# Performance work log

Measured on AMD Instinct MI355X. Metric: run time of the kernel, lower is better.

## Reference

```python
import jax, jax.numpy as jnp
import numpy as np

N_HEAD = 16
RMS_EPS = 1.1920928955078125e-07  # torch float32 finfo eps (F.rms_norm default)


def _apply_rotary(x, cos, sin):
    # x: [B,T,H,D], cos/sin: [1,T,1,D/2]
    d = x.shape[-1] // 2
    x1, x2 = x[..., :d], x[..., d:]
    return jnp.concatenate([x1 * cos + x2 * sin, -x1 * sin + x2 * cos], axis=-1)


def _rms_norm(x):
    var = jnp.mean(jnp.square(x), axis=-1, keepdims=True)
    return x * jax.lax.rsqrt(var + RMS_EPS)


def setup_inputs() -> dict:
    key = jax.random.key(0)
    ks = jax.random.split(key, 5)
    B, T, C, H = 2, 2048, 1024, N_HEAD
    D = C // H
    x = jax.random.normal(ks[0], (B, T, C), dtype=jnp.float32)
    cos = jax.random.uniform(ks[1], (1, T, 1, D // 2), dtype=jnp.float32)
    sin = jax.random.uniform(ks[2], (1, T, 1, D // 2), dtype=jnp.float32)
    kv_w = jax.random.normal(ks[3], (C, C), dtype=jnp.float32) * (C ** -0.5)
    proj_w = jax.random.normal(ks[4], (C, C), dtype=jnp.float32) * (C ** -0.5)
    return {"x": x, "cos": cos, "sin": sin, "kv_w": kv_w, "proj_w": proj_w, "window_left": 1024}


def reference(x, cos, sin, kv_w, proj_w, window_left):
    B, T, C = x.shape
    H = N_HEAD
    D = C // H
    scale = D ** -0.5

    q = x.reshape(B, T, H, D)                       # no Q projection
    kv = (x @ kv_w.T).reshape(B, T, H, D)           # tied K=V projection

    q = _rms_norm(_apply_rotary(q, cos, sin))
    kv = _rms_norm(_apply_rotary(kv, cos, sin))

    # scores: [B,H,T,T]
    scores = jnp.einsum('bqhd,bkhd->bhqk', q, kv) * scale

    pos = jnp.arange(T)
    dist = pos[:, None] - pos[None, :]              # query_pos - key_pos
    allowed = (dist >= 0) & (dist <= window_left)   # causal + sliding window
    scores = jnp.where(allowed[None, None], scores, -jnp.inf)

    attn = jax.nn.softmax(scores, axis=-1)
    out = jnp.einsum('bhqk,bkhd->bqhd', attn, kv).reshape(B, T, C)
    return out @ proj_w.T
```

## Files before the change

### kernel.cpp

```cpp
#include <hip/hip_runtime.h>
#include <hip/hip_bf16.h>

using u16 = unsigned short;
typedef __attribute__((ext_vector_type(8))) short short8v;
typedef __attribute__((ext_vector_type(4))) float f32x4;

#define MFMA16(a, b, c) __builtin_amdgcn_mfma_f32_16x16x32_bf16((a), (b), (c), 0, 0, 0)

#define GLOAD16(g, l) __builtin_amdgcn_global_load_lds(                       \
    (const __attribute__((address_space(1))) void*)(const void*)(g),          \
    (__attribute__((address_space(3))) void*)(void*)(l), 16, 0, 0)

static __device__ __forceinline__ u16 f2bf(float x) {
  __hip_bfloat16 h = __float2bfloat16(x);
  return __builtin_bit_cast(u16, h);
}

__global__ __launch_bounds__(256) void cast_f32_bf16(const float* __restrict__ s,
                                                     u16* __restrict__ d, int n) {
  int i = (blockIdx.x * 256 + threadIdx.x) * 4;
  if (i >= n) return;
  float4 v = *reinterpret_cast<const float4*>(s + i);
  ushort4 o;
  o.x = f2bf(v.x); o.y = f2bf(v.y); o.z = f2bf(v.z); o.w = f2bf(v.w);
  *reinterpret_cast<ushort4*>(d + i) = o;
}

__global__ __launch_bounds__(256) void gemm_bt(const u16* __restrict__ A,
                                               const u16* __restrict__ Bt,
                                               float* __restrict__ C,
                                               int M, int N, int K) {
  __shared__ u16 As[2][64 * 32];
  __shared__ u16 Bs[2][128 * 32];
  unsigned flat = blockIdx.y * gridDim.x + blockIdx.x;
  unsigned nwg = gridDim.x * gridDim.y;
  unsigned swz = (flat & 7) * (nwg >> 3) + (flat >> 3);
  int bm = swz % gridDim.x, bn = swz / gridDim.x;
  int tid = threadIdx.x;
  int wid = tid >> 6, l = tid & 63, lr = l & 15, lg = l >> 4;
  int wr = wid >> 1, wc = wid & 1;

  int srow = l >> 2, scol = (l & 3) * 8;
  const u16* Ag  = A  + (size_t)(bm * 64 + wid * 16 + srow) * K + scol;
  const u16* Bg0 = Bt + (size_t)(bn * 128 + wid * 32 + srow) * K + scol;
  const u16* Bg1 = Bg0 + (size_t)16 * K;

  f32x4 acc[2][4];
#pragma unroll
  for (int m = 0; m < 2; m++)
#pragma unroll
    for (int n = 0; n < 4; n++) acc[m][n] = (f32x4){0.f, 0.f, 0.f, 0.f};

  GLOAD16(Ag, &As[0][wid * 512]);
  GLOAD16(Bg0, &Bs[0][wid * 1024]);
  GLOAD16(Bg1, &Bs[0][wid * 1024 + 512]);
  __syncthreads();

  int cur = 0;
  for (int k0 = 0; k0 < K; k0 += 32) {
    if (k0 + 32 < K) {
      int nb = cur ^ 1;
      GLOAD16(Ag + k0 + 32, &As[nb][wid * 512]);
      GLOAD16(Bg0 + k0 + 32, &Bs[nb][wid * 1024]);
      GLOAD16(Bg1 + k0 + 32, &Bs[nb][wid * 1024 + 512]);
    }

    short8v af[2], bfr[4];
#pragma unroll
    for (int m = 0; m < 2; m++)
      af[m] = *reinterpret_cast<const short8v*>(&As[cur][(wr * 32 + m * 16 + lr) * 32 + lg * 8]);
#pragma unroll
    for (int n = 0; n < 4; n++)
      bfr[n] = *reinterpret_cast<const short8v*>(&Bs[cur][(wc * 64 + n * 16 + lr) * 32 + lg * 8]);
#pragma unroll
    for (int m = 0; m < 2; m++)
#pragma unroll
      for (int n = 0; n < 4; n++) acc[m][n] = MFMA16(af[m], bfr[n], acc[m][n]);

    __syncthreads();
    cur ^= 1;
  }

#pragma unroll
  for (int m = 0; m < 2; m++)
#pragma unroll
    for (int n = 0; n < 4; n++)
#pragma unroll
      for (int r = 0; r < 4; r++) {
        int row = bm * 64 + wr * 32 + m * 16 + lg * 4 + r;
        int col = bn * 128 + wc * 64 + n * 16 + lr;
        C[(size_t)row * N + col] = acc[m][n][r];
      }
}

__global__ __launch_bounds__(256) void rope_rms(const float* __restrict__ src,
                                                u16* __restrict__ dst,
                                                const float* __restrict__ cosp,
                                                const float* __restrict__ sinp,
                                                float scale) {
  int R = blockIdx.x * 4 + (threadIdx.x >> 6);
  int l = threadIdx.x & 63;
  int h = R & 15;
  int bt = R >> 4;
  int t = bt & 2047, b = bt >> 11;

  float v = src[((size_t)R << 6) + l];
  float p = __shfl_xor(v, 32);
  float c = cosp[(t << 5) + (l & 31)];
  float s = sinp[(t << 5) + (l & 31)];
  float r = v * c + ((l < 32) ? p * s : -p * s);
  float sq = r * r;
  sq += __shfl_xor(sq, 32);
  sq += __shfl_xor(sq, 16);
  sq += __shfl_xor(sq, 8);
  sq += __shfl_xor(sq, 4);
  sq += __shfl_xor(sq, 2);
  sq += __shfl_xor(sq, 1);
  float inv = rsqrtf(sq * (1.0f / 64.0f) + 1.1920928955078125e-07f) * scale;
  dst[((((size_t)b * 16 + h) * 2048 + t) << 6) + l] = f2bf(r * inv);
}

__global__ __launch_bounds__(256) void transpose_td(const u16* __restrict__ src,
                                                    u16* __restrict__ dst) {
  __shared__ u16 Ld[64][72];
  int t0 = blockIdx.x << 6, bh = blockIdx.y;
  int tid = threadIdx.x;
#pragma unroll
  for (int i = 0; i < 2; i++) {
    int c = tid + i * 256, tr = c >> 3, sg = c & 7;
    *reinterpret_cast<short8v*>(&Ld[tr][sg * 8]) =
        *reinterpret_cast<const short8v*>(src + ((size_t)bh * 2048 + t0 + tr) * 64 + sg * 8);
  }
  __syncthreads();
#pragma unroll
  for (int i = 0; i < 2; i++) {
    int c = tid + i * 256, dr = c >> 3, sg = c & 7;
    short8v v;
#pragma unroll
    for (int j = 0; j < 8; j++) v[j] = (short)Ld[sg * 8 + j][dr];
    *reinterpret_cast<short8v*>(dst + ((size_t)bh * 64 + dr) * 2048 + t0 + sg * 8) = v;
  }
}

__global__ __launch_bounds__(256) void attn_swa(const u16* __restrict__ Q,
                                                const u16* __restrict__ KV,
                                                const u16* __restrict__ KVt,
                                                u16* __restrict__ O,
                                                const int* __restrict__ winp) {
  const int T = 2048;
  int bid = blockIdx.x;
  int bh = bid & 31;
  int qi = 31 - (bid >> 5);
  int q0 = qi << 6;
  int b = bh >> 4, h = bh & 15;
  int W = *winp;
  int tid = threadIdx.x;
  int wid = tid >> 6, l = tid & 63, lr = l & 15, lg = l >> 4;

  __shared__ u16 Kl[64][72];
  __shared__ u16 Vt[64][72];
  __shared__ u16 Pl[4][16][72];

  const u16* Qb = Q + (((size_t)bh * T + q0 + wid * 16 + lr) << 6);
  short8v aq0 = *reinterpret_cast<const short8v*>(Qb + lg * 8);
  short8v aq1 = *reinterpret_cast<const short8v*>(Qb + 32 + lg * 8);

  const short one_bf = (short)0x3F80;
  short8v vones = {one_bf, one_bf, one_bf, one_bf, one_bf, one_bf, one_bf, one_bf};

  float m_run[4], l_run[4];
  f32x4 oacc[4];
#pragma unroll
  for (int r = 0; r < 4; r++) { m_run[r] = -1e30f; l_run[r] = 0.f; }
#pragma unroll
  for (int dt = 0; dt < 4; dt++) oacc[dt] = (f32x4){0.f, 0.f, 0.f, 0.f};

  int lo = q0 - W;
  if (lo < 0) lo = 0;
  lo &= ~63;

  const u16* KVbh  = KV + (((size_t)bh * T) << 6);
  const u16* KVtbh = KVt + ((size_t)bh << 6) * T;
  int r8 = tid >> 3, sg = tid & 7;

  short8v vK0 = *reinterpret_cast<const short8v*>(KVbh + ((size_t)(lo + r8) << 6) + sg * 8);
  short8v vK1 = *reinterpret_cast<const short8v*>(KVbh + ((size_t)(lo + r8 + 32) << 6) + sg * 8);
  short8v vV0 = *reinterpret_cast<const short8v*>(KVtbh + (size_t)r8 * T + lo + sg * 8);
  short8v vV1 = *reinterpret_cast<const short8v*>(KVtbh + (size_t)(r8 + 32) * T + lo + sg * 8);

  for (int kt = lo; kt <= q0; kt += 64) {
    __syncthreads();
    *reinterpret_cast<short8v*>(&Kl[r8][sg * 8]) = vK0;
    *reinterpret_cast<short8v*>(&Kl[r8 + 32][sg * 8]) = vK1;
    *reinterpret_cast<short8v*>(&Vt[r8][sg * 8]) = vV0;
    *reinterpret_cast<short8v*>(&Vt[r8 + 32][sg * 8]) = vV1;
    __syncthreads();
    if (kt < q0) {
      vK0 = *reinterpret_cast<const short8v*>(KVbh + ((size_t)(kt + 64 + r8) << 6) + sg * 8);
      vK1 = *reinterpret_cast<const short8v*>(KVbh + ((size_t)(kt + 64 + r8 + 32) << 6) + sg * 8);
      vV0 = *reinterpret_cast<const short8v*>(KVtbh + (size_t)r8 * T + kt + 64 + sg * 8);
      vV1 = *reinterpret_cast<const short8v*>(KVtbh + (size_t)(r8 + 32) * T + kt + 64 + sg * 8);
    }

    f32x4 s[4];
#pragma unroll
    for (int nt = 0; nt < 4; nt++) {
      s[nt] = (f32x4){0.f, 0.f, 0.f, 0.f};
      short8v b0 = *reinterpret_cast<const short8v*>(&Kl[nt * 16 + lr][lg * 8]);
      s[nt] = MFMA16(aq0, b0, s[nt]);
      short8v b1 = *reinterpret_cast<const short8v*>(&Kl[nt * 16 + lr][32 + lg * 8]);
      s[nt] = MFMA16(aq1, b1, s[nt]);
    }

    bool edge = (kt + 63 > q0 + wid * 16) || ((q0 - kt) + wid * 16 + 15 > W);

    float al4[4];
#pragma unroll
    for (int r = 0; r < 4; r++) {
      float sv[4], mt;
      if (edge) {
        int t = q0 + wid * 16 + lg * 4 + r;
        mt = -3e38f;
#pragma unroll
        for (int nt = 0; nt < 4; nt++) {
          int k = kt + nt * 16 + lr;
          float val = ((k <= t) && (t - k <= W)) ? s[nt][r] : -3e38f;
          sv[nt] = val;
          mt = fmaxf(mt, val);
        }
      } else {
#pragma unroll
        for (int nt = 0; nt < 4; nt++) sv[nt] = s[nt][r];
        mt = fmaxf(fmaxf(sv[0], sv[1]), fmaxf(sv[2], sv[3]));
      }
      mt = fmaxf(mt, __shfl_xor(mt, 1));
      mt = fmaxf(mt, __shfl_xor(mt, 2));
      mt = fmaxf(mt, __shfl_xor(mt, 4));
      mt = fmaxf(mt, __shfl_xor(mt, 8));
      float mn = fmaxf(m_run[r], mt);
      float al = exp2f(m_run[r] - mn);
      m_run[r] = mn;
      al4[r] = al;
#pragma unroll
      for (int nt = 0; nt < 4; nt++) {
        Pl[wid][lg * 4 + r][nt * 16 + lr] = f2bf(exp2f(sv[nt] - mn));
      }
#pragma unroll
      for (int dt = 0; dt < 4; dt++) oacc[dt][r] *= al;
    }

    short8v ap0 = *reinterpret_cast<const short8v*>(&Pl[wid][lr][lg * 8]);
    short8v ap1 = *reinterpret_cast<const short8v*>(&Pl[wid][lr][32 + lg * 8]);
    f32x4 psum = (f32x4){0.f, 0.f, 0.f, 0.f};
    psum = MFMA16(ap0, vones, psum);
    psum = MFMA16(ap1, vones, psum);
#pragma unroll
    for (int dt = 0; dt < 4; dt++) {
      short8v v0 = *reinterpret_cast<const short8v*>(&Vt[dt * 16 + lr][lg * 8]);
      oacc[dt] = MFMA16(ap0, v0, oacc[dt]);
      short8v v1 = *reinterpret_cast<const short8v*>(&Vt[dt * 16 + lr][32 + lg * 8]);
      oacc[dt] = MFMA16(ap1, v1, oacc[dt]);
    }
#pragma unroll
    for (int r = 0; r < 4; r++) l_run[r] = l_run[r] * al4[r] + psum[r];
  }

#pragma unroll
  for (int r = 0; r < 4; r++) {
    int t = q0 + wid * 16 + lg * 4 + r;
    float inv = 1.f / l_run[r];
#pragma unroll
    for (int dt = 0; dt < 4; dt++) {
      O[(((size_t)b * T + t) << 10) + (h << 6) + dt * 16 + lr] = f2bf(oacc[dt][r] * inv);
    }
  }
}

extern "C" void kernel_launch(void* const* d_in, const int* in_sizes, int n_in,
                              void* d_out, int out_size, void* d_ws, size_t ws_size,
                              hipStream_t stream) {
  (void)in_sizes; (void)n_in; (void)out_size; (void)ws_size;
  const float* x    = (const float*)d_in[0];
  const float* cosp = (const float*)d_in[1];
  const float* sinp = (const float*)d_in[2];
  const float* kvw  = (const float*)d_in[3];
  const float* pw   = (const float*)d_in[4];
  const int*   win  = (const int*)d_in[5];

  char* w = (char*)d_ws;
  u16*   xbf   = (u16*)(w);
  u16*   kvwbf = (u16*)(w + (8u << 20));
  u16*   pwbf  = (u16*)(w + (10u << 20));
  float* kvf   = (float*)(w + (12u << 20));
  u16*   kvt   = (u16*)(w + (12u << 20));
  u16*   aout  = (u16*)(w + (20u << 20));
  u16*   kvbf  = (u16*)(w + (28u << 20));
  u16*   qbf   = xbf;

  cast_f32_bf16<<<4096, 256, 0, stream>>>(x, xbf, 4194304);
  cast_f32_bf16<<<1024, 256, 0, stream>>>(kvw, kvwbf, 1048576);
  cast_f32_bf16<<<1024, 256, 0, stream>>>(pw, pwbf, 1048576);

  gemm_bt<<<dim3(64, 8), 256, 0, stream>>>(xbf, kvwbf, kvf, 4096, 1024, 1024);

  rope_rms<<<16384, 256, 0, stream>>>(x, qbf, cosp, sinp, 0.18033688011112042f);
  rope_rms<<<16384, 256, 0, stream>>>(kvf, kvbf, cosp, sinp, 1.0f);

  transpose_td<<<dim3(32, 32), 256, 0, stream>>>(kvbf, kvt);

  attn_swa<<<1024, 256, 0, stream>>>(qbf, kvbf, kvt, aout, win);

  gemm_bt<<<dim3(64, 8), 256, 0, stream>>>(aout, pwbf, (float*)d_out, 4096, 1024, 1024);
}
```

Baseline: 199.5 us.

## Deepen GEMM LDS pipeline, fuse cast launches, add MFMA priority hints

```diff
diff --git a/kernel.cpp b/kernel.cpp
--- a/kernel.cpp
+++ b/kernel.cpp
@@ -16,22 +16,27 @@
   return __builtin_bit_cast(u16, h);
 }
 
-__global__ __launch_bounds__(256) void cast_f32_bf16(const float* __restrict__ s,
-                                                     u16* __restrict__ d, int n) {
-  int i = (blockIdx.x * 256 + threadIdx.x) * 4;
-  if (i >= n) return;
-  float4 v = *reinterpret_cast<const float4*>(s + i);
+__global__ __launch_bounds__(256) void cast3_f32_bf16(const float* __restrict__ a, u16* __restrict__ da,
+                                                      const float* __restrict__ b, u16* __restrict__ db,
+                                                      const float* __restrict__ c, u16* __restrict__ dc) {
+  int bid = blockIdx.x;
+  const float* s; u16* d; int i;
+  if (bid < 4096)      { s = a; d = da; i = bid; }
+  else if (bid < 5120) { s = b; d = db; i = bid - 4096; }
+  else                 { s = c; d = dc; i = bid - 5120; }
+  int idx = (i * 256 + threadIdx.x) * 4;
+  float4 v = *reinterpret_cast<const float4*>(s + idx);
   ushort4 o;
   o.x = f2bf(v.x); o.y = f2bf(v.y); o.z = f2bf(v.z); o.w = f2bf(v.w);
-  *reinterpret_cast<ushort4*>(d + i) = o;
+  *reinterpret_cast<ushort4*>(d + idx) = o;
 }
 
 __global__ __launch_bounds__(256) void gemm_bt(const u16* __restrict__ A,
                                                const u16* __restrict__ Bt,
                                                float* __restrict__ C,
                                                int M, int N, int K) {
-  __shared__ u16 As[2][64 * 32];
-  __shared__ u16 Bs[2][128 * 32];
+  __shared__ u16 As[4][64 * 32];
+  __shared__ u16 Bs[4][128 * 32];
   unsigned flat = blockIdx.y * gridDim.x + blockIdx.x;
   unsigned nwg = gridDim.x * gridDim.y;
   unsigned swz = (flat & 7) * (nwg >> 3) + (flat >> 3);
@@ -51,19 +56,28 @@
 #pragma unroll
     for (int n = 0; n < 4; n++) acc[m][n] = (f32x4){0.f, 0.f, 0.f, 0.f};
 
-  GLOAD16(Ag, &As[0][wid * 512]);
-  GLOAD16(Bg0, &Bs[0][wid * 1024]);
-  GLOAD16(Bg1, &Bs[0][wid * 1024 + 512]);
-  __syncthreads();
-
-  int cur = 0;
-  for (int k0 = 0; k0 < K; k0 += 32) {
-    if (k0 + 32 < K) {
-      int nb = cur ^ 1;
-      GLOAD16(Ag + k0 + 32, &As[nb][wid * 512]);
-      GLOAD16(Bg0 + k0 + 32, &Bs[nb][wid * 1024]);
-      GLOAD16(Bg1 + k0 + 32, &Bs[nb][wid * 1024 + 512]);
-    }
+  const int NT = K >> 5;
+
+#pragma unroll
+  for (int t = 0; t < 2; t++) {
+    GLOAD16(Ag + t * 32, &As[t][wid * 512]);
+    GLOAD16(Bg0 + t * 32, &Bs[t][wid * 1024]);
+    GLOAD16(Bg1 + t * 32, &Bs[t][wid * 1024 + 512]);
+  }
+
+  for (int t = 0; t < NT; t++) {
+    int cur = t & 3;
+    if (t + 2 < NT) {
+      int nb = (t + 2) & 3;
+      int ko = (t + 2) * 32;
+      GLOAD16(Ag + ko, &As[nb][wid * 512]);
+      GLOAD16(Bg0 + ko, &Bs[nb][wid * 1024]);
+      GLOAD16(Bg1 + ko, &Bs[nb][wid * 1024 + 512]);
+    }
+    if (t + 2 < NT)      asm volatile("s_waitcnt vmcnt(6)" ::: "memory");
+    else if (t + 1 < NT) asm volatile("s_waitcnt vmcnt(3)" ::: "memory");
+    else                 asm volatile("s_waitcnt vmcnt(0)" ::: "memory");
+    __builtin_amdgcn_s_barrier();
 
     short8v af[2], bfr[4];
 #pragma unroll
@@ -72,13 +86,14 @@
 #pragma unroll
     for (int n = 0; n < 4; n++)
       bfr[n] = *reinterpret_cast<const short8v*>(&Bs[cur][(wc * 64 + n * 16 + lr) * 32 + lg * 8]);
+    asm volatile("s_waitcnt lgkmcnt(0)" ::: "memory");
+    __builtin_amdgcn_sched_barrier(0);
+    __builtin_amdgcn_s_setprio(1);
 #pragma unroll
     for (int m = 0; m < 2; m++)
 #pragma unroll
       for (int n = 0; n < 4; n++) acc[m][n] = MFMA16(af[m], bfr[n], acc[m][n]);
-
-    __syncthreads();
-    cur ^= 1;
+    __builtin_amdgcn_s_setprio(0);
   }
 
 #pragma unroll
@@ -203,6 +218,7 @@
     }
 
     f32x4 s[4];
+    __builtin_amdgcn_s_setprio(1);
 #pragma unroll
     for (int nt = 0; nt < 4; nt++) {
       s[nt] = (f32x4){0.f, 0.f, 0.f, 0.f};
@@ -211,6 +227,7 @@
       short8v b1 = *reinterpret_cast<const short8v*>(&Kl[nt * 16 + lr][32 + lg * 8]);
       s[nt] = MFMA16(aq1, b1, s[nt]);
     }
+    __builtin_amdgcn_s_setprio(0);
 
     bool edge = (kt + 63 > q0 + wid * 16) || ((q0 - kt) + wid * 16 + 15 > W);
 
@@ -252,6 +269,7 @@
     short8v ap0 = *reinterpret_cast<const short8v*>(&Pl[wid][lr][lg * 8]);
     short8v ap1 = *reinterpret_cast<const short8v*>(&Pl[wid][lr][32 + lg * 8]);
     f32x4 psum = (f32x4){0.f, 0.f, 0.f, 0.f};
+    __builtin_amdgcn_s_setprio(1);
     psum = MFMA16(ap0, vones, psum);
     psum = MFMA16(ap1, vones, psum);
 #pragma unroll
@@ -261,6 +279,7 @@
       short8v v1 = *reinterpret_cast<const short8v*>(&Vt[dt * 16 + lr][32 + lg * 8]);
       oacc[dt] = MFMA16(ap1, v1, oacc[dt]);
     }
+    __builtin_amdgcn_s_setprio(0);
 #pragma unroll
     for (int r = 0; r < 4; r++) l_run[r] = l_run[r] * al4[r] + psum[r];
   }
@@ -297,9 +316,7 @@
   u16*   kvbf  = (u16*)(w + (28u << 20));
   u16*   qbf   = xbf;
 
-  cast_f32_bf16<<<4096, 256, 0, stream>>>(x, xbf, 4194304);
-  cast_f32_bf16<<<1024, 256, 0, stream>>>(kvw, kvwbf, 1048576);
-  cast_f32_bf16<<<1024, 256, 0, stream>>>(pw, pwbf, 1048576);
+  cast3_f32_bf16<<<6144, 256, 0, stream>>>(x, xbf, kvw, kvwbf, pw, pwbf);
 
   gemm_bt<<<dim3(64, 8), 256, 0, stream>>>(xbf, kvwbf, kvf, 4096, 1024, 1024);
 
```

After: 201.4 us. Within noise of the previous version (+1.0%).
